# Optimization experiments

Measured on AMD Instinct MI355X. Metric: run time of the kernel, lower is better.

The kernel has to match this reference:

```python
import jax, jax.numpy as jnp
import numpy as np
from jax import lax

T = 50
THETA = 1.0 - 0.0001  # max_1 - 0.0001, max_1 = T_win/T = 1.0


def conv_t(x, w, b, pad_h):
    # x: [N, C, H, W, T]; slayer conv3d has time-kernel 1 -> conv2d per timestep.
    n, c, h, wd, t = x.shape
    xb = jnp.moveaxis(x, -1, 1).reshape(n * t, c, h, wd)
    y = lax.conv_general_dilated(xb, w, (1, 1), [(pad_h, pad_h), (0, 0)])
    y = y + b[None, :, None, None]
    o, h2, w2 = y.shape[1], y.shape[2], y.shape[3]
    return jnp.moveaxis(y.reshape(n, t, o, h2, w2), 1, -1)


def if_spikes(a):
    # catCuda.getSpikes on an input stacked T times: IF neuron with constant
    # drive a per step, soft reset (v -= theta on spike). a: [N,C,H,W].
    def step(v, _):
        v = v + a
        s = (v >= THETA).astype(a.dtype)
        return v - s * THETA, s
    _, sp = lax.scan(step, jnp.zeros_like(a), None, length=T)
    return jnp.moveaxis(sp, 0, -1)  # [N,C,H,W,T]


def setup_inputs() -> dict:
    key = jax.random.key(0)
    ks = jax.random.split(key, 6)
    def w(k, shape, scale):
        return jax.random.normal(k, shape, jnp.float32) * scale
    x = jax.random.uniform(ks[0], (256, 1, 180, 1, T), jnp.float32)
    return {
        'x': x,
        'w1': w(ks[1], (16, 1, 3, 1), 0.3), 'b1': jnp.zeros(16, jnp.float32),
        'w2': w(ks[2], (32, 16, 9, 1), 0.1), 'b2': jnp.zeros(32, jnp.float32),
        'w3': w(ks[3], (32, 32, 7, 1), 0.1), 'b3': jnp.zeros(32, jnp.float32),
        'wf': w(ks[4], (4, 32, 83, 1), 0.05), 'bf': jnp.zeros(4, jnp.float32),
    }


def reference(x, w1, b1, w2, b2, w3, b3, wf, bf):
    y = conv_t(x, w1, b1, 1)                        # [N,16,180,1,T]
    y = if_spikes(jnp.sum(y, axis=4) / T)           # rate -> spikes
    y = conv_t(y, w2, b2, 1)                        # [N,32,174,1,T]
    y = if_spikes(jnp.sum(y, axis=4) / T)
    y = 1.1 * (y[:, :, 0::2] + y[:, :, 1::2])       # slayer sum-pool (2,1), weight 1.1
    y = if_spikes(jnp.sum(y, axis=4) / T)           # [N,32,87,1,T]
    y = conv_t(y, w3, b3, 1)                        # [N,32,83,1,T]
    y = if_spikes(jnp.sum(y, axis=4) / T)
    out = jnp.einsum('nchwt,ochw->not', y, wf) + bf[None, :, None]  # dense over full spatial
    return jnp.sum(out, axis=-1) / T                # sum_spikes / T -> [N,4]
```

## Files before the change

### kernel.cpp

```cpp
#include <hip/hip_runtime.h>


#define T_STEPS 50
#define THETA   0.9999f

__device__ __forceinline__ float spike_rate(float a) {
    constexpr float INV = 50.0f / 0.9999f;
    float t = a * INV;
    float c = fminf(fmaxf(floorf(t), 0.0f), 50.0f);
    bool risky = (t > 0.5f) && (fabsf(t - rintf(t)) < 5e-4f);
    if (__ballot(risky)) {
        float v = 0.f, cnt = 0.f;
#pragma unroll 1
        for (int k = 0; k < T_STEPS; ++k) {
            v += a;
            float s = (v >= THETA) ? 1.0f : 0.0f;
            v -= s * THETA;
            cnt += s;
        }
        c = cnt;
    }
    return c / 50.0f;
}

extern "C" __global__ void __launch_bounds__(1024)
catnet_kernel(const float* __restrict__ x,
              const float* __restrict__ w1, const float* __restrict__ b1,
              const float* __restrict__ w2, const float* __restrict__ b2,
              const float* __restrict__ w3, const float* __restrict__ b3,
              const float* __restrict__ wf, const float* __restrict__ bf,
              float* __restrict__ out)
{
    const int n    = blockIdx.x;
    const int tid  = threadIdx.x;
    const int wave = tid >> 6;
    const int lane = tid & 63;

    __shared__ float xbar[182];
    __shared__ float r1p[16][182];
    __shared__ float r2s[32][174];
    __shared__ float r3p[32][89];
    __shared__ float r4s[32][83];
    __shared__ float part[16];

    if (tid < 16)              { r1p[tid][0] = 0.f; r1p[tid][181] = 0.f; }
    if (tid >= 32 && tid < 64) { r3p[tid-32][0] = 0.f; r3p[tid-32][88] = 0.f; }
    if (tid == 64)             { xbar[0] = 0.f; xbar[181] = 0.f; }

    const float* xn = x + (size_t)n * (180 * 50);
    if (tid < 720) {
        const int h = tid >> 2, q = tid & 3;
        const float* row = xn + h * 50;
        float s = 0.f;
        for (int t = q; t < T_STEPS; t += 4) s += row[t];
        s += __shfl_xor(s, 1, 4);
        s += __shfl_xor(s, 2, 4);
        if (q == 0) xbar[h + 1] = s;
    }
    __syncthreads();

    for (int idx = tid; idx < 16 * 180; idx += 1024) {
        int c = idx / 180, h = idx - c * 180;
        float a = w1[c*3+0] * xbar[h] + w1[c*3+1] * xbar[h+1] + w1[c*3+2] * xbar[h+2];
        a = a / 50.0f + b1[c];
        r1p[c][h + 1] = spike_rate(a);
    }
    __syncthreads();

    {
        const int ucg   = __builtin_amdgcn_readfirstlane(wave >> 1);
        const int half  = wave & 1;
        const int hbase = half * 87;
        const int h0 = hbase + lane;
        const int h1 = hbase + 64 + lane;
        const bool v1 = lane < 23;
        const int h1r = v1 ? h1 : h0;
        const float* wb = w2 + ucg * 4 * 144;

        float a[8];
#pragma unroll
        for (int j = 0; j < 4; ++j) { a[j] = b2[ucg*4 + j]; a[4+j] = a[j]; }

        for (int ci = 0; ci < 16; ++ci) {
            float r0[9], r1v[9];
#pragma unroll
            for (int kh = 0; kh < 9; ++kh) {
                r0[kh]  = r1p[ci][h0 + kh];
                r1v[kh] = r1p[ci][h1r + kh];
            }
#pragma unroll
            for (int j = 0; j < 4; ++j) {
                const float* wj = wb + j * 144 + ci * 9;
#pragma unroll
                for (int kh = 0; kh < 9; ++kh) {
                    float wv = wj[kh];
                    a[j]   += wv * r0[kh];
                    a[4+j] += wv * r1v[kh];
                }
            }
        }
#pragma unroll
        for (int j = 0; j < 4; ++j) {
            r2s[ucg*4 + j][h0] = spike_rate(a[j]);
            float rj = spike_rate(a[4+j]);
            if (v1) r2s[ucg*4 + j][h1] = rj;
        }
    }
    __syncthreads();

    for (int idx = tid; idx < 32 * 87; idx += 1024) {
        int c = idx / 87, h = idx - c * 87;
        float a = 1.1f * (r2s[c][2*h] + r2s[c][2*h + 1]);
        r3p[c][h + 1] = spike_rate(a);
    }
    __syncthreads();

    {
        const int ucg   = __builtin_amdgcn_readfirstlane(wave >> 1);
        const int half  = wave & 1;
        const int hbase = half * 42;
        const int cnt   = half ? 41 : 42;
        const bool v0   = lane < cnt;
        const int h0    = hbase + (v0 ? lane : 0);
        const float* wb = w3 + ucg * 4 * 224;

        float a[4];
#pragma unroll
        for (int j = 0; j < 4; ++j) a[j] = b3[ucg*4 + j];

        for (int ci = 0; ci < 32; ++ci) {
            float rv[7];
#pragma unroll
            for (int kh = 0; kh < 7; ++kh) rv[kh] = r3p[ci][h0 + kh];
#pragma unroll
            for (int j = 0; j < 4; ++j) {
                const float* wj = wb + j * 224 + ci * 7;
#pragma unroll
                for (int kh = 0; kh < 7; ++kh)
                    a[j] += wj[kh] * rv[kh];
            }
        }
#pragma unroll
        for (int j = 0; j < 4; ++j) {
            float rj = spike_rate(a[j]);
            if (v0) r4s[ucg*4 + j][h0] = rj;
        }
    }
    __syncthreads();

    {
        const int o = wave >> 2, q = wave & 3;
        const float* r4f = &r4s[0][0];
        const float* wo  = wf + o * (32 * 83);
        float acc = 0.f;
        for (int j = q * 64 + lane; j < 32 * 83; j += 256)
            acc += r4f[j] * wo[j];
#pragma unroll
        for (int off = 32; off > 0; off >>= 1)
            acc += __shfl_down(acc, off, 64);
        if (lane == 0) part[wave] = acc;
    }
    __syncthreads();
    if (tid < 4) {
        float s = part[tid*4] + part[tid*4+1] + part[tid*4+2] + part[tid*4+3];
        out[n * 4 + tid] = s + bf[tid];
    }
}

extern "C" void kernel_launch(void* const* d_in, const int* in_sizes, int n_in,
                              void* d_out, int out_size, void* d_ws, size_t ws_size,
                              hipStream_t stream) {
    const float* x  = (const float*)d_in[0];
    const float* w1 = (const float*)d_in[1];
    const float* b1 = (const float*)d_in[2];
    const float* w2 = (const float*)d_in[3];
    const float* b2 = (const float*)d_in[4];
    const float* w3 = (const float*)d_in[5];
    const float* b3 = (const float*)d_in[6];
    const float* wf = (const float*)d_in[7];
    const float* bf = (const float*)d_in[8];
    float* outp = (float*)d_out;

    catnet_kernel<<<dim3(256), dim3(1024), 0, stream>>>(
        x, w1, b1, w2, b2, w3, b3, wf, bf, outp);
}
```

Baseline: 105.9 us.

## Transpose spike-rate buffers to channel-minor layout with float4 LDS loads in convs

Stores the layer-1 and pool-layer rate buffers as [h][c] with padded channel stride so the conv stages read four input channels per float4 LDS load. Conv2 is remapped so each wave handles 8 output channels over a 44-row slice instead of 4 channels over two row halves. Convolution loops are fully unrolled over channel groups. This is meant to cut LDS instruction count, at the cost of more registers and strided scalar writes when the buffers are filled.

```diff
diff --git a/kernel.cpp b/kernel.cpp
--- a/kernel.cpp
+++ b/kernel.cpp
@@ -37,15 +37,15 @@
     const int lane = tid & 63;
 
     __shared__ float xbar[182];
-    __shared__ float r1p[16][182];
+    __shared__ float r1t[182][20];
     __shared__ float r2s[32][174];
-    __shared__ float r3p[32][89];
+    __shared__ float r3t[89][36];
     __shared__ float r4s[32][83];
     __shared__ float part[16];
 
-    if (tid < 16)              { r1p[tid][0] = 0.f; r1p[tid][181] = 0.f; }
-    if (tid >= 32 && tid < 64) { r3p[tid-32][0] = 0.f; r3p[tid-32][88] = 0.f; }
-    if (tid == 64)             { xbar[0] = 0.f; xbar[181] = 0.f; }
+    if (tid < 20)               { r1t[0][tid] = 0.f; r1t[181][tid] = 0.f; }
+    if (tid >= 32 && tid < 68)  { r3t[0][tid-32] = 0.f; r3t[88][tid-32] = 0.f; }
+    if (tid == 127)             { xbar[0] = 0.f; xbar[181] = 0.f; }
 
     const float* xn = x + (size_t)n * (180 * 50);
     if (tid < 720) {
@@ -63,47 +63,45 @@
         int c = idx / 180, h = idx - c * 180;
         float a = w1[c*3+0] * xbar[h] + w1[c*3+1] * xbar[h+1] + w1[c*3+2] * xbar[h+2];
         a = a / 50.0f + b1[c];
-        r1p[c][h + 1] = spike_rate(a);
+        r1t[h + 1][c] = spike_rate(a);
     }
     __syncthreads();
 
     {
-        const int ucg   = __builtin_amdgcn_readfirstlane(wave >> 1);
-        const int half  = wave & 1;
-        const int hbase = half * 87;
-        const int h0 = hbase + lane;
-        const int h1 = hbase + 64 + lane;
-        const bool v1 = lane < 23;
-        const int h1r = v1 ? h1 : h0;
-        const float* wb = w2 + ucg * 4 * 144;
+        const int g8  = __builtin_amdgcn_readfirstlane(wave >> 2) * 8;
+        const int q   = wave & 3;
+        const int lim = (q == 3) ? 42 : 44;
+        const bool act = lane < lim;
+        const int h0  = q * 44 + lane;
+        const int hr  = act ? h0 : 0;
 
         float a[8];
 #pragma unroll
-        for (int j = 0; j < 4; ++j) { a[j] = b2[ucg*4 + j]; a[4+j] = a[j]; }
+        for (int j = 0; j < 8; ++j) a[j] = b2[g8 + j];
 
-        for (int ci = 0; ci < 16; ++ci) {
-            float r0[9], r1v[9];
+#pragma unroll
+        for (int c4 = 0; c4 < 4; ++c4) {
+            float rw[9][4];
 #pragma unroll
             for (int kh = 0; kh < 9; ++kh) {
-                r0[kh]  = r1p[ci][h0 + kh];
-                r1v[kh] = r1p[ci][h1r + kh];
+                float4 t = *(const float4*)&r1t[hr + kh][c4 * 4];
+                rw[kh][0] = t.x; rw[kh][1] = t.y; rw[kh][2] = t.z; rw[kh][3] = t.w;
             }
 #pragma unroll
-            for (int j = 0; j < 4; ++j) {
-                const float* wj = wb + j * 144 + ci * 9;
+            for (int j = 0; j < 8; ++j) {
+                const float* wj = w2 + ((g8 + j) * 16 + c4 * 4) * 9;
 #pragma unroll
-                for (int kh = 0; kh < 9; ++kh) {
-                    float wv = wj[kh];
-                    a[j]   += wv * r0[kh];
-                    a[4+j] += wv * r1v[kh];
+                for (int u = 0; u < 4; ++u) {
+#pragma unroll
+                    for (int kh = 0; kh < 9; ++kh)
+                        a[j] += wj[u * 9 + kh] * rw[kh][u];
                 }
             }
         }
 #pragma unroll
-        for (int j = 0; j < 4; ++j) {
-            r2s[ucg*4 + j][h0] = spike_rate(a[j]);
-            float rj = spike_rate(a[4+j]);
-            if (v1) r2s[ucg*4 + j][h1] = rj;
+        for (int j = 0; j < 8; ++j) {
+            float r = spike_rate(a[j]);
+            if (act) r2s[g8 + j][h0] = r;
         }
     }
     __syncthreads();
@@ -111,39 +109,45 @@
     for (int idx = tid; idx < 32 * 87; idx += 1024) {
         int c = idx / 87, h = idx - c * 87;
         float a = 1.1f * (r2s[c][2*h] + r2s[c][2*h + 1]);
-        r3p[c][h + 1] = spike_rate(a);
+        r3t[h + 1][c] = spike_rate(a);
     }
     __syncthreads();
 
     {
-        const int ucg   = __builtin_amdgcn_readfirstlane(wave >> 1);
-        const int half  = wave & 1;
-        const int hbase = half * 42;
-        const int cnt   = half ? 41 : 42;
-        const bool v0   = lane < cnt;
-        const int h0    = hbase + (v0 ? lane : 0);
-        const float* wb = w3 + ucg * 4 * 224;
+        const int g4   = __builtin_amdgcn_readfirstlane(wave >> 1) * 4;
+        const int half = wave & 1;
+        const int cnt  = half ? 41 : 42;
+        const bool act = lane < cnt;
+        const int h0   = half * 42 + lane;
+        const int hr   = act ? h0 : 0;
 
         float a[4];
 #pragma unroll
-        for (int j = 0; j < 4; ++j) a[j] = b3[ucg*4 + j];
+        for (int j = 0; j < 4; ++j) a[j] = b3[g4 + j];
 
-        for (int ci = 0; ci < 32; ++ci) {
-            float rv[7];
 #pragma unroll
-            for (int kh = 0; kh < 7; ++kh) rv[kh] = r3p[ci][h0 + kh];
+        for (int c4 = 0; c4 < 8; ++c4) {
+            float rw[7][4];
+#pragma unroll
+            for (int kh = 0; kh < 7; ++kh) {
+                float4 t = *(const float4*)&r3t[hr + kh][c4 * 4];
+                rw[kh][0] = t.x; rw[kh][1] = t.y; rw[kh][2] = t.z; rw[kh][3] = t.w;
+            }
 #pragma unroll
             for (int j = 0; j < 4; ++j) {
-                const float* wj = wb + j * 224 + ci * 7;
+                const float* wj = w3 + ((g4 + j) * 32 + c4 * 4) * 7;
 #pragma unroll
-                for (int kh = 0; kh < 7; ++kh)
-                    a[j] += wj[kh] * rv[kh];
+                for (int u = 0; u < 4; ++u) {
+#pragma unroll
+                    for (int kh = 0; kh < 7; ++kh)
+                        a[j] += wj[u * 7 + kh] * rw[kh][u];
+                }
             }
         }
 #pragma unroll
         for (int j = 0; j < 4; ++j) {
-            float rj = spike_rate(a[j]);
-            if (v0) r4s[ucg*4 + j][h0] = rj;
+            float r = spike_rate(a[j]);
+            if (act) r4s[g4 + j][h0] = r;
         }
     }
     __syncthreads();
```

After: 251.9 us. +137.8%, slower.

## Fuse conv2 spiking with sum-pool stage and drop r2s shared buffer

Applied to the files above, without the earlier changes.

Conv2 threads now each compute the two adjacent output rows that form one pool pair. Each thread loads a 10-wide window shared by both rows, then applies spike_rate, the 1.1x sum-pool and the next spike_rate in registers, writing straight into r3p. This removes the r2s shared buffer, one pass over shared memory and one __syncthreads. Thread-to-row mapping changes to 128 threads per channel group, 87 of them active, so about a third of the lanes in that stage sit idle.

```diff
diff --git a/kernel.cpp b/kernel.cpp
--- a/kernel.cpp
+++ b/kernel.cpp
@@ -38,7 +38,6 @@
 
     __shared__ float xbar[182];
     __shared__ float r1p[16][182];
-    __shared__ float r2s[32][174];
     __shared__ float r3p[32][89];
     __shared__ float r4s[32][83];
     __shared__ float part[16];
@@ -68,70 +67,59 @@
     __syncthreads();
 
     {
-        const int ucg   = __builtin_amdgcn_readfirstlane(wave >> 1);
-        const int half  = wave & 1;
-        const int hbase = half * 87;
-        const int h0 = hbase + lane;
-        const int h1 = hbase + 64 + lane;
-        const bool v1 = lane < 23;
-        const int h1r = v1 ? h1 : h0;
-        const float* wb = w2 + ucg * 4 * 144;
+        const int g   = __builtin_amdgcn_readfirstlane(tid >> 7);
+        const int p   = tid & 127;
+        const bool act = p < 87;
+        const int pr  = act ? p : 0;
+        const float* wb = w2 + g * 4 * 144;
 
-        float a[8];
+        float a0[4], a1[4];
 #pragma unroll
-        for (int j = 0; j < 4; ++j) { a[j] = b2[ucg*4 + j]; a[4+j] = a[j]; }
+        for (int j = 0; j < 4; ++j) { a0[j] = b2[g*4 + j]; a1[j] = a0[j]; }
 
         for (int ci = 0; ci < 16; ++ci) {
-            float r0[9], r1v[9];
+            float w[10];
 #pragma unroll
-            for (int kh = 0; kh < 9; ++kh) {
-                r0[kh]  = r1p[ci][h0 + kh];
-                r1v[kh] = r1p[ci][h1r + kh];
-            }
+            for (int d = 0; d < 10; ++d)
+                w[d] = r1p[ci][2*pr + d];
 #pragma unroll
             for (int j = 0; j < 4; ++j) {
                 const float* wj = wb + j * 144 + ci * 9;
 #pragma unroll
                 for (int kh = 0; kh < 9; ++kh) {
                     float wv = wj[kh];
-                    a[j]   += wv * r0[kh];
-                    a[4+j] += wv * r1v[kh];
+                    a0[j] += wv * w[kh];
+                    a1[j] += wv * w[kh + 1];
                 }
             }
         }
 #pragma unroll
         for (int j = 0; j < 4; ++j) {
-            r2s[ucg*4 + j][h0] = spike_rate(a[j]);
-            float rj = spike_rate(a[4+j]);
-            if (v1) r2s[ucg*4 + j][h1] = rj;
+            float r20 = spike_rate(a0[j]);
+            float r21 = spike_rate(a1[j]);
+            float r3  = spike_rate(1.1f * (r20 + r21));
+            if (act) r3p[g*4 + j][p + 1] = r3;
         }
     }
     __syncthreads();
 
-    for (int idx = tid; idx < 32 * 87; idx += 1024) {
-        int c = idx / 87, h = idx - c * 87;
-        float a = 1.1f * (r2s[c][2*h] + r2s[c][2*h + 1]);
-        r3p[c][h + 1] = spike_rate(a);
-    }
-    __syncthreads();
-
     {
-        const int ucg   = __builtin_amdgcn_readfirstlane(wave >> 1);
-        const int half  = wave & 1;
-        const int hbase = half * 42;
-        const int cnt   = half ? 41 : 42;
-        const bool v0   = lane < cnt;
-        const int h0    = hbase + (v0 ? lane : 0);
-        const float* wb = w3 + ucg * 4 * 224;
+        const int g4   = __builtin_amdgcn_readfirstlane((wave >> 1) * 4);
+        const int half = wave & 1;
+        const int cnt  = half ? 41 : 42;
+        const bool act = lane < cnt;
+        const int h0   = half * 42 + lane;
+        const int hr   = act ? h0 : 0;
+        const float* wb = w3 + g4 * 224;
 
         float a[4];
 #pragma unroll
-        for (int j = 0; j < 4; ++j) a[j] = b3[ucg*4 + j];
+        for (int j = 0; j < 4; ++j) a[j] = b3[g4 + j];
 
         for (int ci = 0; ci < 32; ++ci) {
             float rv[7];
 #pragma unroll
-            for (int kh = 0; kh < 7; ++kh) rv[kh] = r3p[ci][h0 + kh];
+            for (int kh = 0; kh < 7; ++kh) rv[kh] = r3p[ci][hr + kh];
 #pragma unroll
             for (int j = 0; j < 4; ++j) {
                 const float* wj = wb + j * 224 + ci * 7;
@@ -142,8 +130,8 @@
         }
 #pragma unroll
         for (int j = 0; j < 4; ++j) {
-            float rj = spike_rate(a[j]);
-            if (v0) r4s[ucg*4 + j][h0] = rj;
+            float r = spike_rate(a[j]);
+            if (act) r4s[g4 + j][h0] = r;
         }
     }
     __syncthreads();
```

Measured after the change: 104.3 us. Within noise of the previous version (-1.6%).
